# Kernel optimization log

Hardware: AMD Instinct MI355X
Metric: run time of the kernel (lower is better)

## Reference

```python
import jax, jax.numpy as jnp
import numpy as np

N_NODES = 50000
N_EDGES = 600000
D_FEAT = 128


def setup_inputs() -> dict:
    key = jax.random.key(0)
    ks = jax.random.split(key, 10)
    x = jax.random.normal(ks[0], (N_NODES, D_FEAT), dtype=jnp.float32)
    src = jax.random.randint(ks[1], (N_EDGES,), 0, N_NODES, dtype=jnp.int32)
    dst = jax.random.randint(ks[2], (N_EDGES,), 0, N_NODES, dtype=jnp.int32)
    w1 = jax.random.normal(ks[3], (1, D_FEAT), dtype=jnp.float32) * 0.05
    Wd1 = jax.random.normal(ks[4], (D_FEAT, 64), dtype=jnp.float32) * 0.05
    b1 = jnp.zeros((64,), dtype=jnp.float32)
    w2 = jax.random.normal(ks[5], (1, 64), dtype=jnp.float32) * 0.05
    Wd2 = jax.random.normal(ks[6], (64, 32), dtype=jnp.float32) * 0.05
    b2 = jnp.zeros((32,), dtype=jnp.float32)
    Wout = jax.random.normal(ks[7], (32, 4), dtype=jnp.float32) * 0.05
    bout = jnp.zeros((4,), dtype=jnp.float32)
    return {"x": x, "src": src, "dst": dst, "w1": w1, "Wd1": Wd1, "b1": b1,
            "w2": w2, "Wd2": Wd2, "b2": b2, "Wout": Wout, "bout": bout}


def _spmm(src, dst, h):
    # A @ h for COO adjacency (edge src -> dst contributes h[src] into row dst)
    return jax.ops.segment_sum(h[src], dst, num_segments=N_NODES)


def reference(x, src, dst, w1, Wd1, b1, w2, Wd2, b2, Wout, bout):
    # input_layer is an Input wrapper: identity. Dropout is identity at inference.
    h = _spmm(src, dst, x) * w1          # GraphLayer 1: SpMM + elementwise scale
    h = h @ Wd1 + b1                     # Dense(64), linear activation
    h = _spmm(src, dst, h) * w2          # GraphLayer 2
    h = h @ Wd2 + b2                     # Dense(32)
    logits = h @ Wout + bout             # Dense(4)
    return jax.nn.softmax(logits, axis=-1)
```

## Files before the change

### kernel.cpp

```cpp
#include <hip/hip_runtime.h>
#include <hip/hip_bf16.h>

#define D_FEAT 128
#define NP 64
#define NP_SHIFT 6
#define P_PARTS 782
#define CAP 1024
#define EPB 3072
#define XW_BLOCKS 196
#define BK_BLOCKS 196


__global__ __launch_bounds__(256) void fused_xw_bucket_kernel(
    const float4* __restrict__ x4,
    const int* __restrict__ src, const int* __restrict__ dst,
    const float* __restrict__ w1, const float* __restrict__ Wd1,
    const float* __restrict__ b1, const float* __restrict__ w2,
    const float* __restrict__ Wd2, const float* __restrict__ b2,
    const float* __restrict__ Wout, const float* __restrict__ bout,
    int* __restrict__ partFill, int* __restrict__ edgeBuf,
    float* __restrict__ gc, float4* __restrict__ u4, int nN, int nE)
{
    __shared__ int sm[2 * P_PARTS];
    int t = threadIdx.x, b = blockIdx.x;

    if (b < XW_BLOCKS) {
        float* T2   = (float*)sm;
        float* Wall = (float*)sm + 256;
        {
            int m = t >> 2, j = t & 3;
            float s = 0.f;
            for (int p = 0; p < 32; ++p) s += Wd2[m * 32 + p] * Wout[p * 4 + j];
            T2[t] = w2[m] * s;
        }
        __syncthreads();
        for (int idx = t; idx < 512; idx += 256) {
            int k = idx >> 2, j = idx & 3;
            float s = 0.f;
            for (int m = 0; m < 64; ++m) s += Wd1[k * 64 + m] * T2[m * 4 + j];
            Wall[idx] = w1[k] * s;
        }
        if (b == 0 && t < 4) {
            float s = 0.f;
            for (int m = 0; m < 64; ++m) s += b1[m] * T2[m * 4 + t];
            gc[t] = s;
            float s2 = 0.f;
            for (int p = 0; p < 32; ++p) s2 += b2[p] * Wout[p * 4 + t];
            gc[4 + t] = s2 + bout[t];
        }
        __syncthreads();
        int r = b * 256 + t;
        if (r < nN) {
            const float4* W = (const float4*)Wall;
            float4 acc = make_float4(0.f, 0.f, 0.f, 0.f);
            #pragma unroll 8
            for (int k4 = 0; k4 < 32; ++k4) {
                float4 xv = x4[(size_t)r * 32 + k4];
                float4 a0 = W[4 * k4 + 0];
                float4 a1 = W[4 * k4 + 1];
                float4 a2 = W[4 * k4 + 2];
                float4 a3 = W[4 * k4 + 3];
                acc.x += xv.x * a0.x + xv.y * a1.x + xv.z * a2.x + xv.w * a3.x;
                acc.y += xv.x * a0.y + xv.y * a1.y + xv.z * a2.y + xv.w * a3.y;
                acc.z += xv.x * a0.z + xv.y * a1.z + xv.z * a2.z + xv.w * a3.z;
                acc.w += xv.x * a0.w + xv.y * a1.w + xv.z * a2.w + xv.w * a3.w;
            }
            u4[r] = acc;
        }
    } else {
        int bb = b - XW_BLOCKS;
        int* hist = sm;
        int* base = sm + P_PARTS;
        for (int p = t; p < P_PARTS; p += 256) hist[p] = 0;
        __syncthreads();
        const int4* dst4 = (const int4*)dst;
        const int4* src4 = (const int4*)src;
        int nE4  = nE >> 2;
        int b4   = bb * (EPB / 4);
        int end4 = min(b4 + EPB / 4, nE4);
        int4 da[3], sa[3];
        bool va[3];
        #pragma unroll
        for (int it = 0; it < 3; ++it) {
            int i = b4 + it * 256 + t;
            va[it] = i < end4;
            if (va[it]) { da[it] = dst4[i]; sa[it] = src4[i]; }
        }
        #pragma unroll
        for (int it = 0; it < 3; ++it) {
            if (va[it]) {
                atomicAdd(&hist[da[it].x >> NP_SHIFT], 1);
                atomicAdd(&hist[da[it].y >> NP_SHIFT], 1);
                atomicAdd(&hist[da[it].z >> NP_SHIFT], 1);
                atomicAdd(&hist[da[it].w >> NP_SHIFT], 1);
            }
        }
        __syncthreads();
        for (int p = t; p < P_PARTS; p += 256) {
            int h = hist[p];
            base[p] = h ? atomicAdd(&partFill[p], h) : 0;
        }
        __syncthreads();
        auto place = [&](int d, int s) {
            int p = d >> NP_SHIFT;
            int rank = atomicSub(&hist[p], 1) - 1;
            int pos = base[p] + rank;
            if (pos < CAP)
                edgeBuf[p * CAP + pos] = s | ((d & (NP - 1)) << 16);
        };
        #pragma unroll
        for (int it = 0; it < 3; ++it) {
            if (va[it]) {
                place(da[it].x, sa[it].x);
                place(da[it].y, sa[it].y);
                place(da[it].z, sa[it].z);
                place(da[it].w, sa[it].w);
            }
        }
    }
}

__global__ __launch_bounds__(256) void spmm_kernel(
    const int* __restrict__ partFill, const int* __restrict__ edgeBuf,
    const float4* __restrict__ in4, const float* __restrict__ gc, int gcOff,
    float4* __restrict__ out4, int nN, int doSoftmax)
{
    __shared__ float acc[4 * 4 * NP];
    int t = threadIdx.x, p = blockIdx.x;
    acc[t] = 0.f; acc[t + 256] = 0.f; acc[t + 512] = 0.f; acc[t + 768] = 0.f;
    __syncthreads();
    float* my = acc + (t >> 6) * (4 * NP);
    int n = min(partFill[p], CAP);
    const int4* eb4 = (const int4*)(edgeBuf + p * CAP);
    int i0 = t * 4;
    if (i0 < n) {
        int4 e4 = eb4[t];
        int ne = n - i0;
        float4 v0 = in4[e4.x & 0xFFFF];
        float4 v1 = (ne > 1) ? in4[e4.y & 0xFFFF] : make_float4(0, 0, 0, 0);
        float4 v2 = (ne > 2) ? in4[e4.z & 0xFFFF] : make_float4(0, 0, 0, 0);
        float4 v3 = (ne > 3) ? in4[e4.w & 0xFFFF] : make_float4(0, 0, 0, 0);
        int d0 = e4.x >> 16, d1 = e4.y >> 16, d2 = e4.z >> 16, d3 = e4.w >> 16;
        atomicAdd(&my[0 * NP + d0], v0.x);
        atomicAdd(&my[1 * NP + d0], v0.y);
        atomicAdd(&my[2 * NP + d0], v0.z);
        atomicAdd(&my[3 * NP + d0], v0.w);
        if (ne > 1) {
            atomicAdd(&my[0 * NP + d1], v1.x);
            atomicAdd(&my[1 * NP + d1], v1.y);
            atomicAdd(&my[2 * NP + d1], v1.z);
            atomicAdd(&my[3 * NP + d1], v1.w);
        }
        if (ne > 2) {
            atomicAdd(&my[0 * NP + d2], v2.x);
            atomicAdd(&my[1 * NP + d2], v2.y);
            atomicAdd(&my[2 * NP + d2], v2.z);
            atomicAdd(&my[3 * NP + d2], v2.w);
        }
        if (ne > 3) {
            atomicAdd(&my[0 * NP + d3], v3.x);
            atomicAdd(&my[1 * NP + d3], v3.y);
            atomicAdd(&my[2 * NP + d3], v3.z);
            atomicAdd(&my[3 * NP + d3], v3.w);
        }
    }
    __syncthreads();
    if (t < NP) {
        int node = p * NP + t;
        if (node < nN) {
            float lx = acc[0 * NP + t] + acc[256 + 0 * NP + t]
                     + acc[512 + 0 * NP + t] + acc[768 + 0 * NP + t] + gc[gcOff + 0];
            float ly = acc[1 * NP + t] + acc[256 + 1 * NP + t]
                     + acc[512 + 1 * NP + t] + acc[768 + 1 * NP + t] + gc[gcOff + 1];
            float lz = acc[2 * NP + t] + acc[256 + 2 * NP + t]
                     + acc[512 + 2 * NP + t] + acc[768 + 2 * NP + t] + gc[gcOff + 2];
            float lw = acc[3 * NP + t] + acc[256 + 3 * NP + t]
                     + acc[512 + 3 * NP + t] + acc[768 + 3 * NP + t] + gc[gcOff + 3];
            if (doSoftmax) {
                float m = fmaxf(fmaxf(lx, ly), fmaxf(lz, lw));
                float ex = __expf(lx - m);
                float ey = __expf(ly - m);
                float ez = __expf(lz - m);
                float ew = __expf(lw - m);
                float r = 1.f / (ex + ey + ez + ew);
                out4[node] = make_float4(ex * r, ey * r, ez * r, ew * r);
            } else {
                out4[node] = make_float4(lx, ly, lz, lw);
            }
        }
    }
}

extern "C" void kernel_launch(void* const* d_in, const int* in_sizes, int n_in,
                              void* d_out, int out_size, void* d_ws, size_t ws_size,
                              hipStream_t stream)
{
    const float4* x4  = (const float4*)d_in[0];
    const int* srcp   = (const int*)d_in[1];
    const int* dstp   = (const int*)d_in[2];
    const float* w1p  = (const float*)d_in[3];
    const float* Wd1p = (const float*)d_in[4];
    const float* b1p  = (const float*)d_in[5];
    const float* w2p  = (const float*)d_in[6];
    const float* Wd2p = (const float*)d_in[7];
    const float* b2p  = (const float*)d_in[8];
    const float* Woutp = (const float*)d_in[9];
    const float* boutp = (const float*)d_in[10];

    int nE = in_sizes[1];
    int nN = in_sizes[0] / D_FEAT;

    float* ws = (float*)d_ws;
    float* gcp = ws;
    float* u   = ws + 16;
    float* v   = u + (size_t)nN * 4;
    int* partFill = (int*)(v + (size_t)nN * 4);
    int* edgeBuf  = partFill + 1024;
    float4* u4p = (float4*)u;
    float4* v4p = (float4*)v;
    float4* o4  = (float4*)d_out;

    hipMemsetAsync(partFill, 0, P_PARTS * sizeof(int), stream);
    fused_xw_bucket_kernel<<<XW_BLOCKS + BK_BLOCKS, 256, 0, stream>>>(
        x4, srcp, dstp, w1p, Wd1p, b1p, w2p, Wd2p, b2p, Woutp, boutp,
        partFill, edgeBuf, gcp, u4p, nN, nE);
    spmm_kernel<<<P_PARTS, 256, 0, stream>>>(partFill, edgeBuf, u4p,
                                             gcp, 0, v4p, nN, 0);
    spmm_kernel<<<P_PARTS, 256, 0, stream>>>(partFill, edgeBuf, v4p,
                                             gcp, 4, o4, nN, 1);
}
```

Measured before the change: 145.4 us.

## Replace global-atomic bucketing with per-block slot buffers and prefix scan in SpMM

Bucketing now uses 64 blocks that each write edges into private fixed-size slots per partition, using only shared-memory atomics. This removes the global atomicAdd on partFill, the second placement pass and the memset. Each SpMM block scans the per-block counts with wave shuffles and binary-searches to find its edges, and it accumulates into a single shared accumulator instead of four replicas. The risks are silent edge loss if any block gets more than 40 edges for one partition, fewer blocks doing the bucketing, and more shared-atomic contention in SpMM.

```diff
diff --git a/kernel.cpp b/kernel.cpp
--- a/kernel.cpp
+++ b/kernel.cpp
@@ -5,10 +5,10 @@
 #define NP 64
 #define NP_SHIFT 6
 #define P_PARTS 782
-#define CAP 1024
-#define EPB 3072
+#define BK_BLOCKS 64
+#define SLOTS 40
 #define XW_BLOCKS 196
-#define BK_BLOCKS 196
+#define CAPN 1024
 
 
 __global__ __launch_bounds__(256) void fused_xw_bucket_kernel(
@@ -18,10 +18,10 @@
     const float* __restrict__ b1, const float* __restrict__ w2,
     const float* __restrict__ Wd2, const float* __restrict__ b2,
     const float* __restrict__ Wout, const float* __restrict__ bout,
-    int* __restrict__ partFill, int* __restrict__ edgeBuf,
+    int* __restrict__ cnt, int* __restrict__ edgeBuf,
     float* __restrict__ gc, float4* __restrict__ u4, int nN, int nE)
 {
-    __shared__ int sm[2 * P_PARTS];
+    __shared__ int sm[P_PARTS];
     int t = threadIdx.x, b = blockIdx.x;
 
     if (b < XW_BLOCKS) {
@@ -70,112 +70,110 @@
     } else {
         int bb = b - XW_BLOCKS;
         int* hist = sm;
-        int* base = sm + P_PARTS;
         for (int p = t; p < P_PARTS; p += 256) hist[p] = 0;
         __syncthreads();
         const int4* dst4 = (const int4*)dst;
         const int4* src4 = (const int4*)src;
         int nE4  = nE >> 2;
-        int b4   = bb * (EPB / 4);
-        int end4 = min(b4 + EPB / 4, nE4);
-        int4 da[3], sa[3];
-        bool va[3];
-        #pragma unroll
-        for (int it = 0; it < 3; ++it) {
-            int i = b4 + it * 256 + t;
-            va[it] = i < end4;
-            if (va[it]) { da[it] = dst4[i]; sa[it] = src4[i]; }
-        }
-        #pragma unroll
-        for (int it = 0; it < 3; ++it) {
-            if (va[it]) {
-                atomicAdd(&hist[da[it].x >> NP_SHIFT], 1);
-                atomicAdd(&hist[da[it].y >> NP_SHIFT], 1);
-                atomicAdd(&hist[da[it].z >> NP_SHIFT], 1);
-                atomicAdd(&hist[da[it].w >> NP_SHIFT], 1);
+        int c4   = (nE4 + BK_BLOCKS - 1) / BK_BLOCKS;
+        int beg4 = bb * c4;
+        int end4 = min(beg4 + c4, nE4);
+        for (int i = beg4 + t; i < end4; i += 256) {
+            int4 d4 = dst4[i];
+            int4 s4 = src4[i];
+            #pragma unroll
+            for (int k = 0; k < 4; ++k) {
+                int d = (k == 0) ? d4.x : (k == 1) ? d4.y : (k == 2) ? d4.z : d4.w;
+                int s = (k == 0) ? s4.x : (k == 1) ? s4.y : (k == 2) ? s4.z : s4.w;
+                int p = d >> NP_SHIFT;
+                int slot = atomicAdd(&hist[p], 1);
+                if (slot < SLOTS)
+                    edgeBuf[(p * BK_BLOCKS + bb) * SLOTS + slot] =
+                        s | ((d & (NP - 1)) << 16);
             }
         }
         __syncthreads();
-        for (int p = t; p < P_PARTS; p += 256) {
-            int h = hist[p];
-            base[p] = h ? atomicAdd(&partFill[p], h) : 0;
-        }
-        __syncthreads();
-        auto place = [&](int d, int s) {
-            int p = d >> NP_SHIFT;
-            int rank = atomicSub(&hist[p], 1) - 1;
-            int pos = base[p] + rank;
-            if (pos < CAP)
-                edgeBuf[p * CAP + pos] = s | ((d & (NP - 1)) << 16);
-        };
-        #pragma unroll
-        for (int it = 0; it < 3; ++it) {
-            if (va[it]) {
-                place(da[it].x, sa[it].x);
-                place(da[it].y, sa[it].y);
-                place(da[it].z, sa[it].z);
-                place(da[it].w, sa[it].w);
-            }
-        }
+        for (int p = t; p < P_PARTS; p += 256)
+            cnt[bb * P_PARTS + p] = min(hist[p], SLOTS);
     }
 }
 
 __global__ __launch_bounds__(256) void spmm_kernel(
-    const int* __restrict__ partFill, const int* __restrict__ edgeBuf,
+    const int* __restrict__ cnt, const int* __restrict__ edgeBuf,
     const float4* __restrict__ in4, const float* __restrict__ gc, int gcOff,
     float4* __restrict__ out4, int nN, int doSoftmax)
 {
-    __shared__ float acc[4 * 4 * NP];
+    __shared__ int   off[BK_BLOCKS + 1];
+    __shared__ float acc[4 * NP];
     int t = threadIdx.x, p = blockIdx.x;
-    acc[t] = 0.f; acc[t + 256] = 0.f; acc[t + 512] = 0.f; acc[t + 768] = 0.f;
+    acc[t] = 0.f;
+    if (t < BK_BLOCKS) {
+        int v = cnt[t * P_PARTS + p];
+        int inc = v;
+        #pragma unroll
+        for (int s = 1; s < BK_BLOCKS; s <<= 1) {
+            int o = __shfl_up(inc, s, 64);
+            if (t >= s) inc += o;
+        }
+        off[t + 1] = inc;
+        if (t == 0) off[0] = 0;
+    }
     __syncthreads();
-    float* my = acc + (t >> 6) * (4 * NP);
-    int n = min(partFill[p], CAP);
-    const int4* eb4 = (const int4*)(edgeBuf + p * CAP);
+    int n = min(off[BK_BLOCKS], CAPN);
     int i0 = t * 4;
     if (i0 < n) {
-        int4 e4 = eb4[t];
-        int ne = n - i0;
-        float4 v0 = in4[e4.x & 0xFFFF];
-        float4 v1 = (ne > 1) ? in4[e4.y & 0xFFFF] : make_float4(0, 0, 0, 0);
-        float4 v2 = (ne > 2) ? in4[e4.z & 0xFFFF] : make_float4(0, 0, 0, 0);
-        float4 v3 = (ne > 3) ? in4[e4.w & 0xFFFF] : make_float4(0, 0, 0, 0);
-        int d0 = e4.x >> 16, d1 = e4.y >> 16, d2 = e4.z >> 16, d3 = e4.w >> 16;
-        atomicAdd(&my[0 * NP + d0], v0.x);
-        atomicAdd(&my[1 * NP + d0], v0.y);
-        atomicAdd(&my[2 * NP + d0], v0.z);
-        atomicAdd(&my[3 * NP + d0], v0.w);
+        int lo = 0, hi = BK_BLOCKS;
+        while (lo + 1 < hi) {
+            int mid = (lo + hi) >> 1;
+            if (off[mid] <= i0) lo = mid; else hi = mid;
+        }
+        int bb = lo;
+        int ne = min(n - i0, 4);
+        int e[4];
+        #pragma unroll
+        for (int k = 0; k < 4; ++k) {
+            if (k < ne) {
+                int i = i0 + k;
+                while (i >= off[bb + 1]) ++bb;
+                e[k] = edgeBuf[(p * BK_BLOCKS + bb) * SLOTS + (i - off[bb])];
+            } else e[k] = 0;
+        }
+        float4 v0 = in4[e[0] & 0xFFFF];
+        float4 v1 = (ne > 1) ? in4[e[1] & 0xFFFF] : make_float4(0, 0, 0, 0);
+        float4 v2 = (ne > 2) ? in4[e[2] & 0xFFFF] : make_float4(0, 0, 0, 0);
+        float4 v3 = (ne > 3) ? in4[e[3] & 0xFFFF] : make_float4(0, 0, 0, 0);
+        int d0 = e[0] >> 16, d1 = e[1] >> 16, d2 = e[2] >> 16, d3 = e[3] >> 16;
+        atomicAdd(&acc[0 * NP + d0], v0.x);
+        atomicAdd(&acc[1 * NP + d0], v0.y);
+        atomicAdd(&acc[2 * NP + d0], v0.z);
+        atomicAdd(&acc[3 * NP + d0], v0.w);
         if (ne > 1) {
-            atomicAdd(&my[0 * NP + d1], v1.x);
-            atomicAdd(&my[1 * NP + d1], v1.y);
-            atomicAdd(&my[2 * NP + d1], v1.z);
-            atomicAdd(&my[3 * NP + d1], v1.w);
+            atomicAdd(&acc[0 * NP + d1], v1.x);
+            atomicAdd(&acc[1 * NP + d1], v1.y);
+            atomicAdd(&acc[2 * NP + d1], v1.z);
+            atomicAdd(&acc[3 * NP + d1], v1.w);
         }
         if (ne > 2) {
-            atomicAdd(&my[0 * NP + d2], v2.x);
-            atomicAdd(&my[1 * NP + d2], v2.y);
-            atomicAdd(&my[2 * NP + d2], v2.z);
-            atomicAdd(&my[3 * NP + d2], v2.w);
+            atomicAdd(&acc[0 * NP + d2], v2.x);
+            atomicAdd(&acc[1 * NP + d2], v2.y);
+            atomicAdd(&acc[2 * NP + d2], v2.z);
+            atomicAdd(&acc[3 * NP + d2], v2.w);
         }
         if (ne > 3) {
-            atomicAdd(&my[0 * NP + d3], v3.x);
-            atomicAdd(&my[1 * NP + d3], v3.y);
-            atomicAdd(&my[2 * NP + d3], v3.z);
-            atomicAdd(&my[3 * NP + d3], v3.w);
+            atomicAdd(&acc[0 * NP + d3], v3.x);
+            atomicAdd(&acc[1 * NP + d3], v3.y);
+            atomicAdd(&acc[2 * NP + d3], v3.z);
+            atomicAdd(&acc[3 * NP + d3], v3.w);
         }
     }
     __syncthreads();
     if (t < NP) {
         int node = p * NP + t;
         if (node < nN) {
-            float lx = acc[0 * NP + t] + acc[256 + 0 * NP + t]
-                     + acc[512 + 0 * NP + t] + acc[768 + 0 * NP + t] + gc[gcOff + 0];
-            float ly = acc[1 * NP + t] + acc[256 + 1 * NP + t]
-                     + acc[512 + 1 * NP + t] + acc[768 + 1 * NP + t] + gc[gcOff + 1];
-            float lz = acc[2 * NP + t] + acc[256 + 2 * NP + t]
-                     + acc[512 + 2 * NP + t] + acc[768 + 2 * NP + t] + gc[gcOff + 2];
-            float lw = acc[3 * NP + t] + acc[256 + 3 * NP + t]
-                     + acc[512 + 3 * NP + t] + acc[768 + 3 * NP + t] + gc[gcOff + 3];
+            float lx = acc[0 * NP + t] + gc[gcOff + 0];
+            float ly = acc[1 * NP + t] + gc[gcOff + 1];
+            float lz = acc[2 * NP + t] + gc[gcOff + 2];
+            float lw = acc[3 * NP + t] + gc[gcOff + 3];
             if (doSoftmax) {
                 float m = fmaxf(fmaxf(lx, ly), fmaxf(lz, lw));
                 float ex = __expf(lx - m);
@@ -214,18 +212,17 @@
     float* gcp = ws;
     float* u   = ws + 16;
     float* v   = u + (size_t)nN * 4;
-    int* partFill = (int*)(v + (size_t)nN * 4);
-    int* edgeBuf  = partFill + 1024;
+    int* cnt     = (int*)(v + (size_t)nN * 4);
+    int* edgeBuf = cnt + BK_BLOCKS * P_PARTS;
     float4* u4p = (float4*)u;
     float4* v4p = (float4*)v;
     float4* o4  = (float4*)d_out;
 
-    hipMemsetAsync(partFill, 0, P_PARTS * sizeof(int), stream);
     fused_xw_bucket_kernel<<<XW_BLOCKS + BK_BLOCKS, 256, 0, stream>>>(
         x4, srcp, dstp, w1p, Wd1p, b1p, w2p, Wd2p, b2p, Woutp, boutp,
-        partFill, edgeBuf, gcp, u4p, nN, nE);
-    spmm_kernel<<<P_PARTS, 256, 0, stream>>>(partFill, edgeBuf, u4p,
+        cnt, edgeBuf, gcp, u4p, nN, nE);
+    spmm_kernel<<<P_PARTS, 256, 0, stream>>>(cnt, edgeBuf, u4p,
                                              gcp, 0, v4p, nN, 0);
-    spmm_kernel<<<P_PARTS, 256, 0, stream>>>(partFill, edgeBuf, v4p,
+    spmm_kernel<<<P_PARTS, 256, 0, stream>>>(cnt, edgeBuf, v4p,
                                              gcp, 4, o4, nN, 1);
 }
```

Result: no change. 146.9 us (+1.0%).
